# Performance work log

Measured on AMD Instinct MI355X. Metric: run time of the kernel, lower is better.

The kernel has to match this reference:

```python
import jax, jax.numpy as jnp
import numpy as np
from jax.scipy.stats import norm

B, S, D, E, K = 16, 512, 768, 16, 4
NOISE_EPS = 0.01
LOSS_COEF = 0.01


def setup_inputs() -> dict:
    key = jax.random.key(0)
    ks = jax.random.split(key, 6)
    x = jax.random.normal(ks[0], (B, S, D), dtype=jnp.float32)
    noise = jax.random.normal(ks[1], (B, E), dtype=jnp.float32)
    w_gate = jax.random.normal(ks[2], (D, E), dtype=jnp.float32) * 0.02
    w_noise = jax.random.normal(ks[3], (D, E), dtype=jnp.float32) * 0.02
    # initialize_sInit: log(1/(n_experts-1))
    sparse_threshold = jnp.full((1, 1), np.log(1.0 / (E - 1)), dtype=jnp.float32)
    weight = jax.random.normal(ks[4], (E, D, D), dtype=jnp.float32) * 0.02
    bias = jax.random.normal(ks[5], (E, D), dtype=jnp.float32) * 0.02
    return {"x": x, "noise": noise, "w_gate": w_gate, "w_noise": w_noise,
            "sparse_threshold": sparse_threshold, "weight": weight, "bias": bias}


def _cv_squared(v):
    v = v.astype(jnp.float32)
    return jnp.var(v, ddof=1) / (jnp.mean(v) ** 2 + 1e-10)


def reference(x, noise, w_gate, w_noise, sparse_threshold, weight, bias):
    # ---- str_gating (training path, noise supplied externally) ----
    xm = x.mean(axis=1)                                 # [B, D]
    clean_logits = xm @ w_gate                          # [B, E]
    noise_stddev = jax.nn.softplus(xm @ w_noise) + NOISE_EPS
    noisy_logits = clean_logits + noise * noise_stddev  # [B, E]
    gates = jax.nn.softmax(noisy_logits, axis=1)
    # sparseFunction: sign(g) * relu(|g| - sigmoid(s))
    gates = jnp.sign(gates) * jax.nn.relu(jnp.abs(gates) - jax.nn.sigmoid(sparse_threshold))
    # ---- load via _prob_in_top_k (k < n_experts, noisy gating, train) ----
    top_vals = jax.lax.top_k(noisy_logits, K + 1)[0]    # [B, K+1]
    thr_in = top_vals[:, K:K + 1]                       # (k+1)-th largest
    thr_out = top_vals[:, K - 1:K]                      # k-th largest
    is_in = noisy_logits > thr_in
    prob_in = norm.cdf((clean_logits - thr_in) / noise_stddev)
    prob_out = norm.cdf((clean_logits - thr_out) / noise_stddev)
    load = jnp.where(is_in, prob_in, prob_out).sum(axis=0)   # [E]
    importance = gates.sum(axis=0)                      # [E]
    loss = (_cv_squared(importance) + _cv_squared(load)) * LOSS_COEF
    # ---- per-example expert weight mixing (torch broadcasts [B,E,O,I]; same math) ----
    expert_weights = jnp.einsum('be,eoi->boi', gates, weight)  # [B, O, I]
    expert_bias = jnp.einsum('be,eo->bo', gates, bias)         # [B, O]
    # ---- batched matmul: einsum('bij,bkj->bik') ----
    y = jnp.einsum('bsi,boi->bso', x, expert_weights) + expert_bias[:, None, :]
    return y, loss
```

## Files before the change

### kernel.cpp

```cpp
#include <hip/hip_runtime.h>
#include <hip/hip_bf16.h>

#define B_ 16
#define S_ 512
#define D_ 768
#define E_ 16
#define K_ 4

typedef __attribute__((ext_vector_type(8))) short short8;
typedef __attribute__((ext_vector_type(4))) float f32x4;

#define GLOAD16(gp, lp)                                             \
    __builtin_amdgcn_global_load_lds(                               \
        (const __attribute__((address_space(1))) void*)(gp),        \
        (__attribute__((address_space(3))) void*)(lp), 16, 0, 0)

__global__ void k1_mean_cvt(const float* __restrict__ x, __hip_bfloat16* __restrict__ xb,
                            float* __restrict__ partial) {
    int t  = threadIdx.x;
    int b  = blockIdx.x;
    int sc = blockIdx.y;
    size_t rowbase = ((size_t)b * S_ + (size_t)sc * 32) * D_ + t * 4;

    float4 acc = make_float4(0.f, 0.f, 0.f, 0.f);
    #pragma unroll 8
    for (int s = 0; s < 32; ++s) {
        float4 v = *(const float4*)(x + rowbase + (size_t)s * D_);
        acc.x += v.x; acc.y += v.y; acc.z += v.z; acc.w += v.w;
        __hip_bfloat16 h0 = __float2bfloat16(v.x);
        __hip_bfloat16 h1 = __float2bfloat16(v.y);
        __hip_bfloat16 h2 = __float2bfloat16(v.z);
        __hip_bfloat16 h3 = __float2bfloat16(v.w);
        ushort4 pk;
        pk.x = *(unsigned short*)&h0; pk.y = *(unsigned short*)&h1;
        pk.z = *(unsigned short*)&h2; pk.w = *(unsigned short*)&h3;
        *(ushort4*)((unsigned short*)xb + rowbase + (size_t)s * D_) = pk;
    }
    *(float4*)(partial + ((size_t)sc * B_ + b) * D_ + t * 4) = acc;
}

__global__ void k2a_logits(const float* __restrict__ partial,
                           const float* __restrict__ noise,
                           const float* __restrict__ w_gate,
                           const float* __restrict__ w_noise,
                           const float* __restrict__ thr_ptr,
                           float* __restrict__ gates_out,
                           float* __restrict__ clean_out,
                           float* __restrict__ std_out,
                           float* __restrict__ noisy_out,
                           float* __restrict__ thrin_out,
                           float* __restrict__ throut_out) {
    __shared__ float xm[D_];
    __shared__ float red[2][16][17];
    __shared__ float s_noisy[E_];

    int b = blockIdx.x, t = threadIdx.x;

    for (int d = t; d < D_; d += 256) {
        float s = 0.f;
        #pragma unroll
        for (int c = 0; c < 16; ++c) s += partial[((size_t)c * B_ + b) * D_ + d];
        xm[d] = s * (1.0f / S_);
    }
    __syncthreads();

    int e = t & 15, sl = t >> 4;
    const float* wg = w_gate  + (size_t)sl * 48 * E_ + e;
    const float* wn = w_noise + (size_t)sl * 48 * E_ + e;
    float cl = 0.f, nz = 0.f;
    #pragma unroll
    for (int i = 0; i < 48; ++i) {
        float xv = xm[sl * 48 + i];
        cl += xv * wg[(size_t)i * E_];
        nz += xv * wn[(size_t)i * E_];
    }
    red[0][sl][e] = cl;
    red[1][sl][e] = nz;
    __syncthreads();

    if (t < E_) {
        float c2 = 0.f, n2 = 0.f;
        #pragma unroll
        for (int s2 = 0; s2 < 16; ++s2) { c2 += red[0][s2][t]; n2 += red[1][s2][t]; }
        float sp     = fmaxf(n2, 0.f) + log1pf(expf(-fabsf(n2)));
        float stddev = sp + 0.01f;
        float ny     = c2 + noise[b * E_ + t] * stddev;
        s_noisy[t] = ny;
        clean_out[b * E_ + t] = c2;
        std_out[b * E_ + t]   = stddev;
        noisy_out[b * E_ + t] = ny;
    }
    __syncthreads();

    if (t < E_) {
        float ny = s_noisy[t];
        int rank = 0;
        #pragma unroll
        for (int j = 0; j < E_; ++j) {
            float vj = s_noisy[j];
            if (vj > ny || (vj == ny && j < t)) rank++;
        }
        if (rank == K_)     thrin_out[b]  = ny;
        if (rank == K_ - 1) throut_out[b] = ny;

        float mx = -1e30f;
        #pragma unroll
        for (int j = 0; j < E_; ++j) mx = fmaxf(mx, s_noisy[j]);
        float den = 0.f;
        #pragma unroll
        for (int j = 0; j < E_; ++j) den += expf(s_noisy[j] - mx);
        float gate = expf(ny - mx) / den;
        float sig  = 1.f / (1.f + expf(-thr_ptr[0]));
        gates_out[b * E_ + t] = fmaxf(gate - sig, 0.f);
    }
}

__global__ void k3_wb(const float* __restrict__ gates, const float* __restrict__ weight,
                      const float* __restrict__ bias,
                      const float* __restrict__ clean,
                      const float* __restrict__ stdv,
                      const float* __restrict__ noisyv,
                      const float* __restrict__ thrin,
                      const float* __restrict__ throut,
                      __hip_bfloat16* __restrict__ wb, float* __restrict__ ebias,
                      float* __restrict__ loss_out) {
    __shared__ float g[B_ * E_];
    int t = threadIdx.x;
    g[t] = gates[t];
    __syncthreads();

    if (blockIdx.x == 624) {
        __shared__ float s_imp[E_], s_load[E_];
        if (t < E_) {
            float imp = 0.f, ld = 0.f;
            #pragma unroll
            for (int bb = 0; bb < B_; ++bb) {
                imp += g[bb * E_ + t];
                float ti = thrin[bb], to = throut[bb];
                float c2 = clean[bb * E_ + t], sd = stdv[bb * E_ + t], nl = noisyv[bb * E_ + t];
                float z  = (nl > ti) ? (c2 - ti) / sd : (c2 - to) / sd;
                ld += 0.5f * erfcf(-z * 0.70710678118654752f);
            }
            s_imp[t]  = imp;
            s_load[t] = ld;
        }
        __syncthreads();
        if (t == 0) {
            float m1 = 0.f, m2 = 0.f;
            #pragma unroll
            for (int j = 0; j < E_; ++j) { m1 += s_imp[j]; m2 += s_load[j]; }
            m1 /= E_; m2 /= E_;
            float v1 = 0.f, v2 = 0.f;
            #pragma unroll
            for (int j = 0; j < E_; ++j) {
                float a = s_imp[j]  - m1; v1 += a * a;
                float c = s_load[j] - m2; v2 += c * c;
            }
            v1 /= (E_ - 1); v2 /= (E_ - 1);
            loss_out[0] = (v1 / (m1 * m1 + 1e-10f) + v2 / (m2 * m2 + 1e-10f)) * 0.01f;
        }
        return;
    }

    if (blockIdx.x >= 576) {
        int idx = (blockIdx.x - 576) * 256 + t;
        int b = idx / D_, o = idx % D_;
        float acc = 0.f;
        #pragma unroll
        for (int e = 0; e < E_; ++e) acc += g[b * E_ + e] * bias[e * D_ + o];
        ebias[idx] = acc;
        return;
    }

    size_t base = ((size_t)blockIdx.x * 256 + t) * 4;
    float4 acc[B_];
    #pragma unroll
    for (int b = 0; b < B_; ++b) acc[b] = make_float4(0.f, 0.f, 0.f, 0.f);

    #pragma unroll
    for (int e = 0; e < E_; ++e) {
        float4 w4 = *(const float4*)(weight + (size_t)e * D_ * D_ + base);
        #pragma unroll
        for (int b = 0; b < B_; ++b) {
            float ge = g[b * E_ + e];
            acc[b].x += ge * w4.x; acc[b].y += ge * w4.y;
            acc[b].z += ge * w4.z; acc[b].w += ge * w4.w;
        }
    }
    #pragma unroll
    for (int b = 0; b < B_; ++b) {
        __hip_bfloat16 h0 = __float2bfloat16(acc[b].x);
        __hip_bfloat16 h1 = __float2bfloat16(acc[b].y);
        __hip_bfloat16 h2 = __float2bfloat16(acc[b].z);
        __hip_bfloat16 h3 = __float2bfloat16(acc[b].w);
        ushort4 pk;
        pk.x = *(unsigned short*)&h0; pk.y = *(unsigned short*)&h1;
        pk.z = *(unsigned short*)&h2; pk.w = *(unsigned short*)&h3;
        *(ushort4*)((unsigned short*)wb + (size_t)b * D_ * D_ + base) = pk;
    }
}

#define BM 128
#define BN 192
#define BK 64
#define NT (D_ / BK)
#define NBUF 3

__global__ __launch_bounds__(512) void k4_gemm(const __hip_bfloat16* __restrict__ xb,
                                               const __hip_bfloat16* __restrict__ wbm,
                                               const float* __restrict__ ebias,
                                               float* __restrict__ y) {
    extern __shared__ __hip_bfloat16 smem[];
    __hip_bfloat16* As = smem;
    __hip_bfloat16* Bs = smem + NBUF * BM * BK;
    #define AS(buf, r, c) As[((buf) * BM + (r)) * BK + (c)]
    #define BS(buf, r, c) Bs[((buf) * BN + (r)) * BK + (c)]

    int t = threadIdx.x;
    int wgid  = blockIdx.x;
    int xcd   = wgid & 7;
    int local = wgid >> 3;
    int b  = (xcd << 1) | (local & 1);
    int r2 = local >> 1;
    int bm = r2 & 3;
    int bn = r2 >> 2;

    const __hip_bfloat16* xp = xb  + (size_t)b * S_ * D_ + (size_t)(bm * BM) * D_;
    const __hip_bfloat16* wp = wbm + (size_t)b * D_ * D_ + (size_t)(bn * BN) * D_;

    int wave = t >> 6, lane = t & 63;
    int wm = wave >> 2, wn = wave & 3;
    int lrow = lane & 15;
    int lk   = (lane >> 4) << 3;
    int swz  = (lrow & 7) << 3;

    int lr  = lane >> 3;
    int lcs = (((lane & 7) ^ lr) << 3);

    f32x4 zero4 = {0.f, 0.f, 0.f, 0.f};
    f32x4 acc[4][3];
    #pragma unroll
    for (int m = 0; m < 4; ++m)
        #pragma unroll
        for (int n = 0; n < 3; ++n) acc[m][n] = zero4;

    #define STAGE(buf, k0)                                                          \
        do {                                                                        \
            _Pragma("unroll")                                                       \
            for (int i = 0; i < 2; ++i) {                                           \
                int r = wave * 16 + i * 8;                                          \
                GLOAD16(xp + (size_t)(r + lr) * D_ + (k0) + lcs, &AS(buf, r, 0));   \
            }                                                                       \
            _Pragma("unroll")                                                       \
            for (int i = 0; i < 3; ++i) {                                           \
                int r = wave * 24 + i * 8;                                          \
                GLOAD16(wp + (size_t)(r + lr) * D_ + (k0) + lcs, &BS(buf, r, 0));   \
            }                                                                       \
        } while (0)

    #define COMPUTE(buf)                                                            \
        do {                                                                        \
            _Pragma("unroll")                                                       \
            for (int kk = 0; kk < BK; kk += 32) {                                   \
                short8 afr[4], bfr[3];                                              \
                _Pragma("unroll")                                                   \
                for (int m = 0; m < 4; ++m)                                         \
                    afr[m] = *(const short8*)(&AS(buf, wm * 64 + m * 16 + lrow,     \
                                                  (kk + lk) ^ swz));                \
                _Pragma("unroll")                                                   \
                for (int n = 0; n < 3; ++n)                                         \
                    bfr[n] = *(const short8*)(&BS(buf, wn * 48 + n * 16 + lrow,     \
                                                  (kk + lk) ^ swz));                \
                _Pragma("unroll")                                                   \
                for (int m = 0; m < 4; ++m)                                         \
                    _Pragma("unroll")                                               \
                    for (int n = 0; n < 3; ++n)                                     \
                        acc[m][n] = __builtin_amdgcn_mfma_f32_16x16x32_bf16(        \
                            afr[m], bfr[n], acc[m][n], 0, 0, 0);                    \
            }                                                                       \
        } while (0)

    STAGE(0, 0);
    STAGE(1, BK);
    asm volatile("s_waitcnt vmcnt(5)" ::: "memory");
    __builtin_amdgcn_s_barrier();
    __builtin_amdgcn_sched_barrier(0);

    #pragma unroll
    for (int kt = 0; kt < NT; ++kt) {
        if (kt + 2 < NT) STAGE((kt + 2) % NBUF, (kt + 2) * BK);
        __builtin_amdgcn_s_setprio(1);
        COMPUTE(kt % NBUF);
        __builtin_amdgcn_s_setprio(0);
        if (kt + 1 < NT) {
            if (kt + 2 < NT) asm volatile("s_waitcnt vmcnt(5)" ::: "memory");
            else             asm volatile("s_waitcnt vmcnt(0)" ::: "memory");
            __builtin_amdgcn_s_barrier();
            __builtin_amdgcn_sched_barrier(0);
        }
    }

    float* yp = y + (size_t)b * S_ * D_ + (size_t)(bm * BM) * D_ + bn * BN;
    const float* ep = ebias + (size_t)b * D_ + bn * BN;
    int crow = (lane >> 4) * 4;
    int ccol = lane & 15;
    #pragma unroll
    for (int n = 0; n < 3; ++n) {
        float eb = ep[wn * 48 + n * 16 + ccol];
        #pragma unroll
        for (int m = 0; m < 4; ++m) {
            #pragma unroll
            for (int j = 0; j < 4; ++j) {
                yp[(size_t)(wm * 64 + m * 16 + crow + j) * D_ + wn * 48 + n * 16 + ccol] =
                    acc[m][n][j] + eb;
            }
        }
    }
    #undef STAGE
    #undef COMPUTE
    #undef AS
    #undef BS
}

extern "C" void kernel_launch(void* const* d_in, const int* in_sizes, int n_in,
                              void* d_out, int out_size, void* d_ws, size_t ws_size,
                              hipStream_t stream) {
    const float* x       = (const float*)d_in[0];
    const float* noise   = (const float*)d_in[1];
    const float* w_gate  = (const float*)d_in[2];
    const float* w_noise = (const float*)d_in[3];
    const float* thr     = (const float*)d_in[4];
    const float* weight  = (const float*)d_in[5];
    const float* bias    = (const float*)d_in[6];
    float* out = (float*)d_out;

    char* ws = (char*)d_ws;
    float*          partial = (float*)(ws + 0);
    float*          gates   = (float*)(ws + 786432);
    float*          clean   = (float*)(ws + 787456);
    float*          stdv    = (float*)(ws + 788480);
    float*          noisyv  = (float*)(ws + 789504);
    float*          thrin   = (float*)(ws + 790528);
    float*          throut  = (float*)(ws + 790592);
    float*          ebias   = (float*)(ws + 790656);
    __hip_bfloat16* xb      = (__hip_bfloat16*)(ws + 839808);
    __hip_bfloat16* wb      = (__hip_bfloat16*)(ws + 13422720);

    k1_mean_cvt<<<dim3(B_, 16), 192, 0, stream>>>(x, xb, partial);
    k2a_logits<<<16, 256, 0, stream>>>(partial, noise, w_gate, w_noise, thr, gates,
                                       clean, stdv, noisyv, thrin, throut);
    k3_wb<<<625, 256, 0, stream>>>(gates, weight, bias, clean, stdv, noisyv, thrin, throut,
                                   wb, ebias, out + (size_t)B_ * S_ * D_);
    k4_gemm<<<256, 512, 122880, stream>>>(xb, wb, ebias, out);
}
```

Baseline: 57.44 us.

## Fuse all stages into one cooperative persistent kernel with grid syncs

Replaces the four separate launches (mean/convert, gating logits, weight mixing, GEMM) with a single cooperative kernel of 256 blocks that separates phases with grid.sync. Expert weight loads are issued right after the first sync, so they overlap the gating computation done by the first 16 blocks. This removes launch gaps and inter-kernel drains. In exchange it pays for grid-wide barriers and larger register pressure from 16 float4 weight registers, and the mixing and GEMM phases are now limited to 256 blocks of 512 threads.

```diff
diff --git a/kernel.cpp b/kernel.cpp
--- a/kernel.cpp
+++ b/kernel.cpp
@@ -1,5 +1,8 @@
 #include <hip/hip_runtime.h>
 #include <hip/hip_bf16.h>
+#include <hip/hip_cooperative_groups.h>
+
+namespace cg = cooperative_groups;
 
 #define B_ 16
 #define S_ 512
@@ -9,196 +12,12 @@
 
 typedef __attribute__((ext_vector_type(8))) short short8;
 typedef __attribute__((ext_vector_type(4))) float f32x4;
+typedef __attribute__((ext_vector_type(4))) unsigned short u16x4;
 
 #define GLOAD16(gp, lp)                                             \
     __builtin_amdgcn_global_load_lds(                               \
         (const __attribute__((address_space(1))) void*)(gp),        \
         (__attribute__((address_space(3))) void*)(lp), 16, 0, 0)
-
-__global__ void k1_mean_cvt(const float* __restrict__ x, __hip_bfloat16* __restrict__ xb,
-                            float* __restrict__ partial) {
-    int t  = threadIdx.x;
-    int b  = blockIdx.x;
-    int sc = blockIdx.y;
-    size_t rowbase = ((size_t)b * S_ + (size_t)sc * 32) * D_ + t * 4;
-
-    float4 acc = make_float4(0.f, 0.f, 0.f, 0.f);
-    #pragma unroll 8
-    for (int s = 0; s < 32; ++s) {
-        float4 v = *(const float4*)(x + rowbase + (size_t)s * D_);
-        acc.x += v.x; acc.y += v.y; acc.z += v.z; acc.w += v.w;
-        __hip_bfloat16 h0 = __float2bfloat16(v.x);
-        __hip_bfloat16 h1 = __float2bfloat16(v.y);
-        __hip_bfloat16 h2 = __float2bfloat16(v.z);
-        __hip_bfloat16 h3 = __float2bfloat16(v.w);
-        ushort4 pk;
-        pk.x = *(unsigned short*)&h0; pk.y = *(unsigned short*)&h1;
-        pk.z = *(unsigned short*)&h2; pk.w = *(unsigned short*)&h3;
-        *(ushort4*)((unsigned short*)xb + rowbase + (size_t)s * D_) = pk;
-    }
-    *(float4*)(partial + ((size_t)sc * B_ + b) * D_ + t * 4) = acc;
-}
-
-__global__ void k2a_logits(const float* __restrict__ partial,
-                           const float* __restrict__ noise,
-                           const float* __restrict__ w_gate,
-                           const float* __restrict__ w_noise,
-                           const float* __restrict__ thr_ptr,
-                           float* __restrict__ gates_out,
-                           float* __restrict__ clean_out,
-                           float* __restrict__ std_out,
-                           float* __restrict__ noisy_out,
-                           float* __restrict__ thrin_out,
-                           float* __restrict__ throut_out) {
-    __shared__ float xm[D_];
-    __shared__ float red[2][16][17];
-    __shared__ float s_noisy[E_];
-
-    int b = blockIdx.x, t = threadIdx.x;
-
-    for (int d = t; d < D_; d += 256) {
-        float s = 0.f;
-        #pragma unroll
-        for (int c = 0; c < 16; ++c) s += partial[((size_t)c * B_ + b) * D_ + d];
-        xm[d] = s * (1.0f / S_);
-    }
-    __syncthreads();
-
-    int e = t & 15, sl = t >> 4;
-    const float* wg = w_gate  + (size_t)sl * 48 * E_ + e;
-    const float* wn = w_noise + (size_t)sl * 48 * E_ + e;
-    float cl = 0.f, nz = 0.f;
-    #pragma unroll
-    for (int i = 0; i < 48; ++i) {
-        float xv = xm[sl * 48 + i];
-        cl += xv * wg[(size_t)i * E_];
-        nz += xv * wn[(size_t)i * E_];
-    }
-    red[0][sl][e] = cl;
-    red[1][sl][e] = nz;
-    __syncthreads();
-
-    if (t < E_) {
-        float c2 = 0.f, n2 = 0.f;
-        #pragma unroll
-        for (int s2 = 0; s2 < 16; ++s2) { c2 += red[0][s2][t]; n2 += red[1][s2][t]; }
-        float sp     = fmaxf(n2, 0.f) + log1pf(expf(-fabsf(n2)));
-        float stddev = sp + 0.01f;
-        float ny     = c2 + noise[b * E_ + t] * stddev;
-        s_noisy[t] = ny;
-        clean_out[b * E_ + t] = c2;
-        std_out[b * E_ + t]   = stddev;
-        noisy_out[b * E_ + t] = ny;
-    }
-    __syncthreads();
-
-    if (t < E_) {
-        float ny = s_noisy[t];
-        int rank = 0;
-        #pragma unroll
-        for (int j = 0; j < E_; ++j) {
-            float vj = s_noisy[j];
-            if (vj > ny || (vj == ny && j < t)) rank++;
-        }
-        if (rank == K_)     thrin_out[b]  = ny;
-        if (rank == K_ - 1) throut_out[b] = ny;
-
-        float mx = -1e30f;
-        #pragma unroll
-        for (int j = 0; j < E_; ++j) mx = fmaxf(mx, s_noisy[j]);
-        float den = 0.f;
-        #pragma unroll
-        for (int j = 0; j < E_; ++j) den += expf(s_noisy[j] - mx);
-        float gate = expf(ny - mx) / den;
-        float sig  = 1.f / (1.f + expf(-thr_ptr[0]));
-        gates_out[b * E_ + t] = fmaxf(gate - sig, 0.f);
-    }
-}
-
-__global__ void k3_wb(const float* __restrict__ gates, const float* __restrict__ weight,
-                      const float* __restrict__ bias,
-                      const float* __restrict__ clean,
-                      const float* __restrict__ stdv,
-                      const float* __restrict__ noisyv,
-                      const float* __restrict__ thrin,
-                      const float* __restrict__ throut,
-                      __hip_bfloat16* __restrict__ wb, float* __restrict__ ebias,
-                      float* __restrict__ loss_out) {
-    __shared__ float g[B_ * E_];
-    int t = threadIdx.x;
-    g[t] = gates[t];
-    __syncthreads();
-
-    if (blockIdx.x == 624) {
-        __shared__ float s_imp[E_], s_load[E_];
-        if (t < E_) {
-            float imp = 0.f, ld = 0.f;
-            #pragma unroll
-            for (int bb = 0; bb < B_; ++bb) {
-                imp += g[bb * E_ + t];
-                float ti = thrin[bb], to = throut[bb];
-                float c2 = clean[bb * E_ + t], sd = stdv[bb * E_ + t], nl = noisyv[bb * E_ + t];
-                float z  = (nl > ti) ? (c2 - ti) / sd : (c2 - to) / sd;
-                ld += 0.5f * erfcf(-z * 0.70710678118654752f);
-            }
-            s_imp[t]  = imp;
-            s_load[t] = ld;
-        }
-        __syncthreads();
-        if (t == 0) {
-            float m1 = 0.f, m2 = 0.f;
-            #pragma unroll
-            for (int j = 0; j < E_; ++j) { m1 += s_imp[j]; m2 += s_load[j]; }
-            m1 /= E_; m2 /= E_;
-            float v1 = 0.f, v2 = 0.f;
-            #pragma unroll
-            for (int j = 0; j < E_; ++j) {
-                float a = s_imp[j]  - m1; v1 += a * a;
-                float c = s_load[j] - m2; v2 += c * c;
-            }
-            v1 /= (E_ - 1); v2 /= (E_ - 1);
-            loss_out[0] = (v1 / (m1 * m1 + 1e-10f) + v2 / (m2 * m2 + 1e-10f)) * 0.01f;
-        }
-        return;
-    }
-
-    if (blockIdx.x >= 576) {
-        int idx = (blockIdx.x - 576) * 256 + t;
-        int b = idx / D_, o = idx % D_;
-        float acc = 0.f;
-        #pragma unroll
-        for (int e = 0; e < E_; ++e) acc += g[b * E_ + e] * bias[e * D_ + o];
-        ebias[idx] = acc;
-        return;
-    }
-
-    size_t base = ((size_t)blockIdx.x * 256 + t) * 4;
-    float4 acc[B_];
-    #pragma unroll
-    for (int b = 0; b < B_; ++b) acc[b] = make_float4(0.f, 0.f, 0.f, 0.f);
-
-    #pragma unroll
-    for (int e = 0; e < E_; ++e) {
-        float4 w4 = *(const float4*)(weight + (size_t)e * D_ * D_ + base);
-        #pragma unroll
-        for (int b = 0; b < B_; ++b) {
-            float ge = g[b * E_ + e];
-            acc[b].x += ge * w4.x; acc[b].y += ge * w4.y;
-            acc[b].z += ge * w4.z; acc[b].w += ge * w4.w;
-        }
-    }
-    #pragma unroll
-    for (int b = 0; b < B_; ++b) {
-        __hip_bfloat16 h0 = __float2bfloat16(acc[b].x);
-        __hip_bfloat16 h1 = __float2bfloat16(acc[b].y);
-        __hip_bfloat16 h2 = __float2bfloat16(acc[b].z);
-        __hip_bfloat16 h3 = __float2bfloat16(acc[b].w);
-        ushort4 pk;
-        pk.x = *(unsigned short*)&h0; pk.y = *(unsigned short*)&h1;
-        pk.z = *(unsigned short*)&h2; pk.w = *(unsigned short*)&h3;
-        *(ushort4*)((unsigned short*)wb + (size_t)b * D_ * D_ + base) = pk;
-    }
-}
 
 #define BM 128
 #define BN 192
@@ -206,120 +25,306 @@
 #define NT (D_ / BK)
 #define NBUF 3
 
-__global__ __launch_bounds__(512) void k4_gemm(const __hip_bfloat16* __restrict__ xb,
-                                               const __hip_bfloat16* __restrict__ wbm,
-                                               const float* __restrict__ ebias,
-                                               float* __restrict__ y) {
+__device__ __forceinline__ u16x4 pack_bf16x4(f32x4 v) {
+    u16x4 pk;
+    #pragma unroll
+    for (int i = 0; i < 4; ++i) {
+        __hip_bfloat16 h = __float2bfloat16(v[i]);
+        pk[i] = *(unsigned short*)&h;
+    }
+    return pk;
+}
+
+__device__ __forceinline__ void mix_store(const f32x4* wv, const float* gsm,
+                                          unsigned short* wbp, size_t pos) {
+    #pragma unroll
+    for (int b = 0; b < B_; ++b) {
+        f32x4 a = {0.f, 0.f, 0.f, 0.f};
+        #pragma unroll
+        for (int e = 0; e < E_; ++e) a += gsm[b * E_ + e] * wv[e];
+        *(u16x4*)(wbp + (size_t)b * D_ * D_ + pos * 4) = pack_bf16x4(a);
+    }
+}
+
+__global__ __launch_bounds__(512, 2) void moe_fused(
+    const float* __restrict__ x, const float* __restrict__ noise,
+    const float* __restrict__ w_gate, const float* __restrict__ w_noise,
+    const float* __restrict__ thrp, const float* __restrict__ weight,
+    const float* __restrict__ bias, float* __restrict__ out,
+    float* __restrict__ partial, float* __restrict__ gates_g,
+    float* __restrict__ clean_g, float* __restrict__ stdv_g,
+    float* __restrict__ noisyv_g, float* __restrict__ thrin_g,
+    float* __restrict__ throut_g, float* __restrict__ ebias,
+    __hip_bfloat16* __restrict__ xb, __hip_bfloat16* __restrict__ wb)
+{
     extern __shared__ __hip_bfloat16 smem[];
-    __hip_bfloat16* As = smem;
-    __hip_bfloat16* Bs = smem + NBUF * BM * BK;
-    #define AS(buf, r, c) As[((buf) * BM + (r)) * BK + (c)]
-    #define BS(buf, r, c) Bs[((buf) * BN + (r)) * BK + (c)]
-
-    int t = threadIdx.x;
-    int wgid  = blockIdx.x;
-    int xcd   = wgid & 7;
-    int local = wgid >> 3;
-    int b  = (xcd << 1) | (local & 1);
-    int r2 = local >> 1;
-    int bm = r2 & 3;
-    int bn = r2 >> 2;
-
-    const __hip_bfloat16* xp = xb  + (size_t)b * S_ * D_ + (size_t)(bm * BM) * D_;
-    const __hip_bfloat16* wp = wbm + (size_t)b * D_ * D_ + (size_t)(bn * BN) * D_;
-
-    int wave = t >> 6, lane = t & 63;
-    int wm = wave >> 2, wn = wave & 3;
-    int lrow = lane & 15;
-    int lk   = (lane >> 4) << 3;
-    int swz  = (lrow & 7) << 3;
-
-    int lr  = lane >> 3;
-    int lcs = (((lane & 7) ^ lr) << 3);
-
-    f32x4 zero4 = {0.f, 0.f, 0.f, 0.f};
-    f32x4 acc[4][3];
-    #pragma unroll
-    for (int m = 0; m < 4; ++m)
-        #pragma unroll
-        for (int n = 0; n < 3; ++n) acc[m][n] = zero4;
-
-    #define STAGE(buf, k0)                                                          \
-        do {                                                                        \
-            _Pragma("unroll")                                                       \
-            for (int i = 0; i < 2; ++i) {                                           \
-                int r = wave * 16 + i * 8;                                          \
-                GLOAD16(xp + (size_t)(r + lr) * D_ + (k0) + lcs, &AS(buf, r, 0));   \
-            }                                                                       \
-            _Pragma("unroll")                                                       \
-            for (int i = 0; i < 3; ++i) {                                           \
-                int r = wave * 24 + i * 8;                                          \
-                GLOAD16(wp + (size_t)(r + lr) * D_ + (k0) + lcs, &BS(buf, r, 0));   \
-            }                                                                       \
-        } while (0)
-
-    #define COMPUTE(buf)                                                            \
-        do {                                                                        \
-            _Pragma("unroll")                                                       \
-            for (int kk = 0; kk < BK; kk += 32) {                                   \
-                short8 afr[4], bfr[3];                                              \
-                _Pragma("unroll")                                                   \
-                for (int m = 0; m < 4; ++m)                                         \
-                    afr[m] = *(const short8*)(&AS(buf, wm * 64 + m * 16 + lrow,     \
-                                                  (kk + lk) ^ swz));                \
-                _Pragma("unroll")                                                   \
-                for (int n = 0; n < 3; ++n)                                         \
-                    bfr[n] = *(const short8*)(&BS(buf, wn * 48 + n * 16 + lrow,     \
-                                                  (kk + lk) ^ swz));                \
-                _Pragma("unroll")                                                   \
-                for (int m = 0; m < 4; ++m)                                         \
-                    _Pragma("unroll")                                               \
-                    for (int n = 0; n < 3; ++n)                                     \
-                        acc[m][n] = __builtin_amdgcn_mfma_f32_16x16x32_bf16(        \
-                            afr[m], bfr[n], acc[m][n], 0, 0, 0);                    \
-            }                                                                       \
-        } while (0)
-
-    STAGE(0, 0);
-    STAGE(1, BK);
-    asm volatile("s_waitcnt vmcnt(5)" ::: "memory");
-    __builtin_amdgcn_s_barrier();
-    __builtin_amdgcn_sched_barrier(0);
-
-    #pragma unroll
-    for (int kt = 0; kt < NT; ++kt) {
-        if (kt + 2 < NT) STAGE((kt + 2) % NBUF, (kt + 2) * BK);
-        __builtin_amdgcn_s_setprio(1);
-        COMPUTE(kt % NBUF);
-        __builtin_amdgcn_s_setprio(0);
-        if (kt + 1 < NT) {
-            if (kt + 2 < NT) asm volatile("s_waitcnt vmcnt(5)" ::: "memory");
-            else             asm volatile("s_waitcnt vmcnt(0)" ::: "memory");
-            __builtin_amdgcn_s_barrier();
-            __builtin_amdgcn_sched_barrier(0);
-        }
-    }
-
-    float* yp = y + (size_t)b * S_ * D_ + (size_t)(bm * BM) * D_ + bn * BN;
-    const float* ep = ebias + (size_t)b * D_ + bn * BN;
-    int crow = (lane >> 4) * 4;
-    int ccol = lane & 15;
-    #pragma unroll
-    for (int n = 0; n < 3; ++n) {
-        float eb = ep[wn * 48 + n * 16 + ccol];
-        #pragma unroll
-        for (int m = 0; m < 4; ++m) {
-            #pragma unroll
-            for (int j = 0; j < 4; ++j) {
-                yp[(size_t)(wm * 64 + m * 16 + crow + j) * D_ + wn * 48 + n * 16 + ccol] =
-                    acc[m][n][j] + eb;
-            }
-        }
-    }
-    #undef STAGE
-    #undef COMPUTE
-    #undef AS
-    #undef BS
+    __shared__ float xm[D_];
+    __shared__ float red[2][16][17];
+    __shared__ float s_noisy[E_];
+    __shared__ float gs[B_ * E_];
+    __shared__ float s_imp[E_], s_load[E_];
+
+    cg::grid_group grid = cg::this_grid();
+    const int blk = blockIdx.x, t = threadIdx.x;
+
+    {
+        int b = blk >> 4, sc = blk & 15;
+        if (t < 384) {
+            int d4 = t % 192, half = t / 192;
+            size_t rowbase = ((size_t)b * S_ + sc * 32 + half * 16) * D_ + d4 * 4;
+            f32x4 acc = {0.f, 0.f, 0.f, 0.f};
+            #pragma unroll 4
+            for (int s = 0; s < 16; ++s) {
+                f32x4 v = *(const f32x4*)(x + rowbase + (size_t)s * D_);
+                acc += v;
+                *(u16x4*)((unsigned short*)xb + rowbase + (size_t)s * D_) = pack_bf16x4(v);
+            }
+            *(f32x4*)(partial + ((size_t)(sc * 2 + half) * B_ + b) * D_ + d4 * 4) = acc;
+        }
+    }
+    grid.sync();
+
+    size_t gpos = (size_t)blk * 512 + t;
+    f32x4 wreg[16];
+    if (blk >= 16) {
+        #pragma unroll
+        for (int e = 0; e < E_; ++e)
+            wreg[e] = *(const f32x4*)(weight + (size_t)e * D_ * D_ + gpos * 4);
+    }
+
+    if (blk < 16) {
+        int b = blk;
+        if (t < 256) {
+            for (int d = t; d < D_; d += 256) {
+                float s = 0.f;
+                #pragma unroll
+                for (int c = 0; c < 32; ++c) s += partial[((size_t)c * B_ + b) * D_ + d];
+                xm[d] = s * (1.0f / S_);
+            }
+        }
+        __syncthreads();
+        if (t < 256) {
+            int e = t & 15, sl = t >> 4;
+            const float* wg = w_gate  + (size_t)sl * 48 * E_ + e;
+            const float* wn = w_noise + (size_t)sl * 48 * E_ + e;
+            float cl = 0.f, nz = 0.f;
+            #pragma unroll
+            for (int i = 0; i < 48; ++i) {
+                float xv = xm[sl * 48 + i];
+                cl += xv * wg[(size_t)i * E_];
+                nz += xv * wn[(size_t)i * E_];
+            }
+            red[0][sl][e] = cl;
+            red[1][sl][e] = nz;
+        }
+        __syncthreads();
+        if (t < E_) {
+            float c2 = 0.f, n2 = 0.f;
+            #pragma unroll
+            for (int s2 = 0; s2 < 16; ++s2) { c2 += red[0][s2][t]; n2 += red[1][s2][t]; }
+            float sp     = fmaxf(n2, 0.f) + log1pf(expf(-fabsf(n2)));
+            float stddev = sp + 0.01f;
+            float ny     = c2 + noise[b * E_ + t] * stddev;
+            s_noisy[t] = ny;
+            clean_g[b * E_ + t]  = c2;
+            stdv_g[b * E_ + t]   = stddev;
+            noisyv_g[b * E_ + t] = ny;
+        }
+        __syncthreads();
+        if (t < E_) {
+            float ny = s_noisy[t];
+            int rank = 0;
+            #pragma unroll
+            for (int j = 0; j < E_; ++j) {
+                float vj = s_noisy[j];
+                if (vj > ny || (vj == ny && j < t)) rank++;
+            }
+            if (rank == K_)     thrin_g[b]  = ny;
+            if (rank == K_ - 1) throut_g[b] = ny;
+            float mx = -1e30f;
+            #pragma unroll
+            for (int j = 0; j < E_; ++j) mx = fmaxf(mx, s_noisy[j]);
+            float den = 0.f;
+            #pragma unroll
+            for (int j = 0; j < E_; ++j) den += expf(s_noisy[j] - mx);
+            float gate = expf(ny - mx) / den;
+            float sig  = 1.f / (1.f + expf(-thrp[0]));
+            gates_g[b * E_ + t] = fmaxf(gate - sig, 0.f);
+        }
+    }
+    grid.sync();
+
+    if (t < B_ * E_) gs[t] = gates_g[t];
+    __syncthreads();
+
+    if (blk < 16) {
+        #pragma unroll
+        for (int e = 0; e < E_; ++e)
+            wreg[e] = *(const f32x4*)(weight + (size_t)e * D_ * D_ + gpos * 4);
+    }
+    mix_store(wreg, gs, (unsigned short*)wb, gpos);
+
+    if (blk < 32) {
+        size_t g2 = gpos + 131072;
+        f32x4 w2[16];
+        #pragma unroll
+        for (int e = 0; e < E_; ++e)
+            w2[e] = *(const f32x4*)(weight + (size_t)e * D_ * D_ + g2 * 4);
+        mix_store(w2, gs, (unsigned short*)wb, g2);
+    }
+
+    if (blk >= 32 && blk < 80 && t < 256) {
+        int idx = (blk - 32) * 256 + t;
+        int b = idx / D_, o = idx % D_;
+        float a = 0.f;
+        #pragma unroll
+        for (int e = 0; e < E_; ++e) a += gs[b * E_ + e] * bias[e * D_ + o];
+        ebias[idx] = a;
+    }
+
+    if (blk == 200) {
+        if (t < E_) {
+            float imp = 0.f, ld = 0.f;
+            #pragma unroll
+            for (int bb = 0; bb < B_; ++bb) {
+                imp += gs[bb * E_ + t];
+                float ti = thrin_g[bb], to = throut_g[bb];
+                float c2 = clean_g[bb * E_ + t], sd = stdv_g[bb * E_ + t];
+                float nl = noisyv_g[bb * E_ + t];
+                float z  = (nl > ti) ? (c2 - ti) / sd : (c2 - to) / sd;
+                ld += 0.5f * erfcf(-z * 0.70710678118654752f);
+            }
+            s_imp[t]  = imp;
+            s_load[t] = ld;
+        }
+        __syncthreads();
+        if (t == 0) {
+            float m1 = 0.f, m2 = 0.f;
+            #pragma unroll
+            for (int j = 0; j < E_; ++j) { m1 += s_imp[j]; m2 += s_load[j]; }
+            m1 /= E_; m2 /= E_;
+            float v1 = 0.f, v2 = 0.f;
+            #pragma unroll
+            for (int j = 0; j < E_; ++j) {
+                float a = s_imp[j]  - m1; v1 += a * a;
+                float c = s_load[j] - m2; v2 += c * c;
+            }
+            v1 /= (E_ - 1); v2 /= (E_ - 1);
+            out[(size_t)B_ * S_ * D_] = (v1 / (m1 * m1 + 1e-10f) + v2 / (m2 * m2 + 1e-10f)) * 0.01f;
+        }
+    }
+    grid.sync();
+
+    {
+        __hip_bfloat16* As = smem;
+        __hip_bfloat16* Bs = smem + NBUF * BM * BK;
+        #define AS(buf, r, c) As[((buf) * BM + (r)) * BK + (c)]
+        #define BS(buf, r, c) Bs[((buf) * BN + (r)) * BK + (c)]
+
+        int wgid  = blk;
+        int xcd   = wgid & 7;
+        int local = wgid >> 3;
+        int b  = (xcd << 1) | (local & 1);
+        int r2 = local >> 1;
+        int bm = r2 & 3;
+        int bn = r2 >> 2;
+
+        const __hip_bfloat16* xp = xb + (size_t)b * S_ * D_ + (size_t)(bm * BM) * D_;
+        const __hip_bfloat16* wp = wb + (size_t)b * D_ * D_ + (size_t)(bn * BN) * D_;
+
+        int wave = t >> 6, lane = t & 63;
+        int wm = wave >> 2, wn = wave & 3;
+        int lrow = lane & 15;
+        int lk   = (lane >> 4) << 3;
+        int swz  = (lrow & 7) << 3;
+
+        int lr  = lane >> 3;
+        int lcs = (((lane & 7) ^ lr) << 3);
+
+        f32x4 zero4 = {0.f, 0.f, 0.f, 0.f};
+        f32x4 acc[4][3];
+        #pragma unroll
+        for (int m = 0; m < 4; ++m)
+            #pragma unroll
+            for (int n = 0; n < 3; ++n) acc[m][n] = zero4;
+
+        #define STAGE(buf, k0)                                                          \
+            do {                                                                        \
+                _Pragma("unroll")                                                       \
+                for (int i = 0; i < 2; ++i) {                                           \
+                    int r = wave * 16 + i * 8;                                          \
+                    GLOAD16(xp + (size_t)(r + lr) * D_ + (k0) + lcs, &AS(buf, r, 0));   \
+                }                                                                       \
+                _Pragma("unroll")                                                       \
+                for (int i = 0; i < 3; ++i) {                                           \
+                    int r = wave * 24 + i * 8;                                          \
+                    GLOAD16(wp + (size_t)(r + lr) * D_ + (k0) + lcs, &BS(buf, r, 0));   \
+                }                                                                       \
+            } while (0)
+
+        #define COMPUTE(buf)                                                            \
+            do {                                                                        \
+                _Pragma("unroll")                                                       \
+                for (int kk = 0; kk < BK; kk += 32) {                                   \
+                    short8 afr[4], bfr[3];                                              \
+                    _Pragma("unroll")                                                   \
+                    for (int m = 0; m < 4; ++m)                                         \
+                        afr[m] = *(const short8*)(&AS(buf, wm * 64 + m * 16 + lrow,     \
+                                                      (kk + lk) ^ swz));                \
+                    _Pragma("unroll")                                                   \
+                    for (int n = 0; n < 3; ++n)                                         \
+                        bfr[n] = *(const short8*)(&BS(buf, wn * 48 + n * 16 + lrow,     \
+                                                      (kk + lk) ^ swz));                \
+                    _Pragma("unroll")                                                   \
+                    for (int m = 0; m < 4; ++m)                                         \
+                        _Pragma("unroll")                                               \
+                        for (int n = 0; n < 3; ++n)                                     \
+                            acc[m][n] = __builtin_amdgcn_mfma_f32_16x16x32_bf16(        \
+                                afr[m], bfr[n], acc[m][n], 0, 0, 0);                    \
+                }                                                                       \
+            } while (0)
+
+        STAGE(0, 0);
+        STAGE(1, BK);
+        asm volatile("s_waitcnt vmcnt(5)" ::: "memory");
+        __builtin_amdgcn_s_barrier();
+        __builtin_amdgcn_sched_barrier(0);
+
+        #pragma unroll
+        for (int kt = 0; kt < NT; ++kt) {
+            if (kt + 2 < NT) STAGE((kt + 2) % NBUF, (kt + 2) * BK);
+            __builtin_amdgcn_s_setprio(1);
+            COMPUTE(kt % NBUF);
+            __builtin_amdgcn_s_setprio(0);
+            if (kt + 1 < NT) {
+                if (kt + 2 < NT) asm volatile("s_waitcnt vmcnt(5)" ::: "memory");
+                else             asm volatile("s_waitcnt vmcnt(0)" ::: "memory");
+                __builtin_amdgcn_s_barrier();
+                __builtin_amdgcn_sched_barrier(0);
+            }
+        }
+
+        float* yp = out + (size_t)b * S_ * D_ + (size_t)(bm * BM) * D_ + bn * BN;
+        const float* ep = ebias + (size_t)b * D_ + bn * BN;
+        int crow = (lane >> 4) * 4;
+        int ccol = lane & 15;
+        #pragma unroll
+        for (int n = 0; n < 3; ++n) {
+            float eb = ep[wn * 48 + n * 16 + ccol];
+            #pragma unroll
+            for (int m = 0; m < 4; ++m) {
+                #pragma unroll
+                for (int j = 0; j < 4; ++j) {
+                    yp[(size_t)(wm * 64 + m * 16 + crow + j) * D_ + wn * 48 + n * 16 + ccol] =
+                        acc[m][n][j] + eb;
+                }
+            }
+        }
+        #undef STAGE
+        #undef COMPUTE
+        #undef AS
+        #undef BS
+    }
 }
 
 extern "C" void kernel_launch(void* const* d_in, const int* in_sizes, int n_in,
@@ -336,20 +341,21 @@
 
     char* ws = (char*)d_ws;
     float*          partial = (float*)(ws + 0);
-    float*          gates   = (float*)(ws + 786432);
-    float*          clean   = (float*)(ws + 787456);
-    float*          stdv    = (float*)(ws + 788480);
-    float*          noisyv  = (float*)(ws + 789504);
-    float*          thrin   = (float*)(ws + 790528);
-    float*          throut  = (float*)(ws + 790592);
-    float*          ebias   = (float*)(ws + 790656);
-    __hip_bfloat16* xb      = (__hip_bfloat16*)(ws + 839808);
-    __hip_bfloat16* wb      = (__hip_bfloat16*)(ws + 13422720);
-
-    k1_mean_cvt<<<dim3(B_, 16), 192, 0, stream>>>(x, xb, partial);
-    k2a_logits<<<16, 256, 0, stream>>>(partial, noise, w_gate, w_noise, thr, gates,
-                                       clean, stdv, noisyv, thrin, throut);
-    k3_wb<<<625, 256, 0, stream>>>(gates, weight, bias, clean, stdv, noisyv, thrin, throut,
-                                   wb, ebias, out + (size_t)B_ * S_ * D_);
-    k4_gemm<<<256, 512, 122880, stream>>>(xb, wb, ebias, out);
+    float*          gates   = (float*)(ws + 1572864);
+    float*          clean   = (float*)(ws + 1573888);
+    float*          stdv    = (float*)(ws + 1574912);
+    float*          noisyv  = (float*)(ws + 1575936);
+    float*          thrin   = (float*)(ws + 1576960);
+    float*          throut  = (float*)(ws + 1577024);
+    float*          ebias   = (float*)(ws + 1577088);
+    __hip_bfloat16* xb      = (__hip_bfloat16*)(ws + 1626240);
+    __hip_bfloat16* wb      = (__hip_bfloat16*)(ws + 14209152);
+
+    void* args[] = { (void*)&x, (void*)&noise, (void*)&w_gate, (void*)&w_noise,
+                     (void*)&thr, (void*)&weight, (void*)&bias, (void*)&out,
+                     (void*)&partial, (void*)&gates, (void*)&clean, (void*)&stdv,
+                     (void*)&noisyv, (void*)&thrin, (void*)&throut, (void*)&ebias,
+                     (void*)&xb, (void*)&wb };
+    hipLaunchCooperativeKernel((const void*)moe_fused, dim3(256), dim3(512),
+                               args, 122880, stream);
 }
```

Measured after the change: 158.0 us. +175.1%, slower.
